# Performance work log

Hardware: AMD Instinct MI355X
Metric: run time of the kernel (lower is better)

The kernel has to match this reference:

```python
import jax, jax.numpy as jnp
import numpy as np

ALPHA = 0.1   # leaky integration rate
NOISE = 0.02  # noise std
B, T, I, H, O = 64, 512, 128, 1024, 64


def setup_inputs() -> dict:
    key = jax.random.key(0)
    k1, k2, k3, k4, k5 = jax.random.split(key, 5)
    x = jax.random.normal(k1, (B, T, I), dtype=jnp.float32)
    wi = jax.random.normal(k2, (I, H), dtype=jnp.float32) / np.sqrt(I).astype(np.float32)
    wrec = jax.random.normal(k3, (H, H), dtype=jnp.float32) / np.sqrt(H).astype(np.float32)
    wo = jax.random.normal(k4, (H, O), dtype=jnp.float32) / np.sqrt(H).astype(np.float32)
    noise = jax.random.normal(k5, (B, T, H), dtype=jnp.float32)  # pre-sampled standard normal
    return {"x": x, "noise": noise, "wi": wi, "wrec": wrec, "wo": wo}


def reference(x, noise, wi, wrec, wo):
    # x: [B,T,I], noise: [B,T,H]; leaky tanh RNN scanned over time.
    batch = x.shape[0]
    h0 = jnp.zeros((batch, wrec.shape[0]), dtype=x.dtype)
    xs = jnp.swapaxes(x, 0, 1)       # [T,B,I]
    ns = jnpp if False else jnp.swapaxes(noise, 0, 1)  # [T,B,H]

    def step(h, inp):
        xt, nt = inp
        h = (1.0 - ALPHA) * h + ALPHA * (xt @ wi + jnp.tanh(h) @ wrec + nt * NOISE)
        return h, jnp.tanh(h) @ wo   # per-step output [B,O]

    _, outs = jax.lax.scan(step, h0, (xs, ns))  # outs: [T,B,O]
    return jnp.swapaxes(outs, 0, 1)  # [B,T,O]
```

## Files before the change

### kernel.cpp

```cpp
#include <hip/hip_runtime.h>
#include <hip/hip_bf16.h>


#define T_ 512
#define I_ 128
#define H_ 1024
#define O_ 64
#define GRPS 8
#define BG 8
#define WPG 32
#define NWG 256
#define POLL_CAP (1<<17)

#define GBUF_ELEMS (GRPS*2*BG*H_)
#define GBUF_BYTES (GBUF_ELEMS*2)
#define STEPFLAG_OFF GBUF_BYTES
#define WS_NEED (GBUF_BYTES + 1024)

#define WREC_HI_E 0
#define WREC_LO_E 32768
#define WI_HI_E   65536
#define WI_LO_E   69632
#define WO_HI_E   73728
#define WO_LO_E   75776
#define RED_OFF_B   155648
#define NOISE_OFF_B 160256
#define LDS_BYTES   161280

typedef __bf16 bf16x8 __attribute__((ext_vector_type(8)));
typedef float f32x4 __attribute__((ext_vector_type(4)));
typedef unsigned u32x4 __attribute__((ext_vector_type(4)));
typedef unsigned short u16;

__device__ __forceinline__ float fast_tanh(float v){
  float cx = fminf(fmaxf(v, -14.f), 14.f);
  float e = __builtin_amdgcn_exp2f(cx * 2.8853900817779268f);
  return 1.f - 2.f * __builtin_amdgcn_rcpf(e + 1.f);
}

__device__ __forceinline__ unsigned sflag_load(const u16* p){
  unsigned v;
  asm volatile("global_load_ushort %0, %1, off sc0 sc1\n\ts_waitcnt vmcnt(0)"
               : "=v"(v) : "v"(p) : "memory");
  return v;
}
__device__ __forceinline__ void sflag_store(u16* p, unsigned v){
  asm volatile("global_store_short %0, %1, off sc0 sc1" :: "v"(p), "v"(v) : "memory");
}
__device__ __forceinline__ void g_load_frag(u32x4& d, const u16* p){
  asm volatile("global_load_dwordx4 %0, %1, off sc0 sc1" : "=v"(d) : "v"(p) : "memory");
}
__device__ __forceinline__ void g_store_u16(u16* p, unsigned v){
  asm volatile("global_store_short %0, %1, off sc0 sc1" :: "v"(p), "v"(v) : "memory");
}

__device__ void load_slice(const float* __restrict__ Wg, int ld, int c0, int K,
                           __bf16* hi, __bf16* lo){
  for (int idx = threadIdx.x; idx < K*32; idx += 256){
    int k = idx >> 5, c = idx & 31;
    float v = Wg[(size_t)k*ld + c0 + c];
    __bf16 h = (__bf16)v;
    __bf16 l = (__bf16)(v - (float)h);
    int kt = k >> 5, kin = k & 31, lg = kin >> 3, j = kin & 7;
    int off = (((kt*2 + (c>>4))*64 + (lg*16 + (c&15))) << 3) + j;
    hi[off] = h; lo[off] = l;
  }
}

#define MFMA __builtin_amdgcn_mfma_f32_16x16x32_bf16
#define BC(u) __builtin_bit_cast(bf16x8, u)

extern "C" __global__ __launch_bounds__(256, 1)
void rnn_kernel(const float* __restrict__ x, const float* __restrict__ noise,
                const float* __restrict__ wi, const float* __restrict__ wrec,
                const float* __restrict__ wo, float* __restrict__ out,
                u16* __restrict__ gbuf, u16* __restrict__ sflags)
{
  extern __shared__ char smem[];
  __bf16* B = (__bf16*)smem;
  float* RED = (float*)(smem + RED_OFF_B);
  float* NS  = (float*)(smem + NOISE_OFF_B);

  const int grp  = blockIdx.x >> 5;
  const int role = blockIdx.x & 31;
  const int c0 = role * 32;

  load_slice(wrec, H_, c0, H_, B + WREC_HI_E, B + WREC_LO_E);
  load_slice(wi,   H_, c0, I_, B + WI_HI_E,  B + WI_LO_E);
  for (int idx = threadIdx.x; idx < 2*H_; idx += 256){
    int col = idx >> 10, k = idx & (H_-1);
    float v = wo[(size_t)k*O_ + role*2 + col];
    __bf16 hh = (__bf16)v;
    B[WO_HI_E + col*H_ + k] = hh;
    B[WO_LO_E + col*H_ + k] = (__bf16)(v - (float)hh);
  }
  __syncthreads();

  const int lane = threadIdx.x & 63;
  const int w    = threadIdx.x >> 6;
  const int lhalf = lane >> 4;
  const int l15   = lane & 15;
  const int bf = lane * 8;

  u16* gg = gbuf + grp * (2*BG*H_);
  u16* gf = sflags + grp * 32;
  const u16* pollp = gf + (lane & 31);
  u16* myflag = gf + role;
  const u16* abase = gg + (size_t)(lane & 7)*H_ + w*256 + lhalf*8;
  const int wo_off = (l15 & 1)*1024 + lhalf*8;

  f32x4 h0 = {0.f,0.f,0.f,0.f};
  f32x4 xA = {0.f,0.f,0.f,0.f}, xB = {0.f,0.f,0.f,0.f};

  for (int i = 0; i < T_; ++i){
    if (w < 2){
      xA = (f32x4){0.f,0.f,0.f,0.f}; xB = (f32x4){0.f,0.f,0.f,0.f};
      const float* xp = x + ((size_t)(grp*BG + (l15 & 7))*T_ + i)*I_ + lhalf*8;
      #pragma unroll
      for (int kt = 0; kt < 4; ++kt){
        f32x4 v0 = *(const f32x4*)(xp + kt*32);
        f32x4 v1 = *(const f32x4*)(xp + kt*32 + 4);
        bf16x8 xh, xl;
        #pragma unroll
        for (int j = 0; j < 4; ++j){
          float a = v0[j], b2 = v1[j];
          __bf16 ah = (__bf16)a, bh2 = (__bf16)b2;
          xh[j] = ah; xh[j+4] = bh2;
          xl[j] = (__bf16)(a - (float)ah); xl[j+4] = (__bf16)(b2 - (float)bh2);
        }
        bf16x8 wih = *(const bf16x8*)(B + WI_HI_E + kt*1024 + w*512 + bf);
        bf16x8 wil = *(const bf16x8*)(B + WI_LO_E + kt*1024 + w*512 + bf);
        xA = MFMA(xh, wih, xA, 0,0,0);
        xB = MFMA(xl, wih, xB, 0,0,0);
        xA = MFMA(xh, wil, xA, 0,0,0);
      }
    } else if (w == 3){
      #pragma unroll
      for (int q = 0; q < 4; ++q){
        int b = (lane>>5) + q*2, c = lane & 31;
        NS[b*32 + c] = noise[((size_t)(grp*BG + b)*T_ + i)*H_ + c0 + c];
      }
    }

    if (i > 0){
      const unsigned tgt = (unsigned)i;
      int guard = 0;
      while (true){
        unsigned v = sflag_load(pollp);
        if (__all((int)(v >= tgt))) break;
        if (++guard > POLL_CAP) break;
      }
    }

    const u16* ap = abase + (size_t)(i & 1)*BG*H_;
    u32x4 a[8];
    #pragma unroll
    for (int kt = 0; kt < 8; ++kt) g_load_frag(a[kt], ap + kt*32);
    asm volatile("s_waitcnt vmcnt(0)"
      : "+v"(a[0]),"+v"(a[1]),"+v"(a[2]),"+v"(a[3]),
        "+v"(a[4]),"+v"(a[5]),"+v"(a[6]),"+v"(a[7]));
    __builtin_amdgcn_sched_barrier(0);

    f32x4 c0A={0.f,0.f,0.f,0.f}, c0B={0.f,0.f,0.f,0.f};
    f32x4 c1A={0.f,0.f,0.f,0.f}, c1B={0.f,0.f,0.f,0.f};
    f32x4 oA ={0.f,0.f,0.f,0.f}, oB ={0.f,0.f,0.f,0.f};
    if (w == 0){ c0A = xA; c0B = xB; }
    if (w == 1){ c1A = xA; c1B = xB; }
    const int kb = w*8;
    #pragma unroll
    for (int kt = 0; kt < 8; ++kt){
      const int kg = kb + kt;
      bf16x8 bh0 = *(const bf16x8*)(B + WREC_HI_E + kg*1024 + bf);
      bf16x8 bl0 = *(const bf16x8*)(B + WREC_LO_E + kg*1024 + bf);
      bf16x8 bh1 = *(const bf16x8*)(B + WREC_HI_E + kg*1024 + 512 + bf);
      bf16x8 bl1 = *(const bf16x8*)(B + WREC_LO_E + kg*1024 + 512 + bf);
      bf16x8 wh  = *(const bf16x8*)(B + WO_HI_E + wo_off + kg*32);
      bf16x8 wl  = *(const bf16x8*)(B + WO_LO_E + wo_off + kg*32);
      bf16x8 av = BC(a[kt]);
      c0A = MFMA(av, bh0, c0A, 0,0,0);  c0B = MFMA(av, bl0, c0B, 0,0,0);
      c1A = MFMA(av, bh1, c1A, 0,0,0);  c1B = MFMA(av, bl1, c1B, 0,0,0);
      oA  = MFMA(av, wh,  oA,  0,0,0);  oB  = MFMA(av, wl,  oB,  0,0,0);
    }
    f32x4 cn0 = c0A + c0B, cn1 = c1A + c1B, co = oA + oB;

    if (lane < 32){
      if (w == 0){ *(f32x4*)&RED[((1*3+0)*32+lane)*4] = cn1; *(f32x4*)&RED[((2*3+0)*32+lane)*4] = co; }
      if (w == 1){ *(f32x4*)&RED[((0*3+0)*32+lane)*4] = cn0; *(f32x4*)&RED[((2*3+1)*32+lane)*4] = co; }
      if (w == 2){ *(f32x4*)&RED[((0*3+1)*32+lane)*4] = cn0; *(f32x4*)&RED[((1*3+1)*32+lane)*4] = cn1; }
      if (w == 3){ *(f32x4*)&RED[((0*3+2)*32+lane)*4] = cn0; *(f32x4*)&RED[((1*3+2)*32+lane)*4] = cn1; *(f32x4*)&RED[((2*3+2)*32+lane)*4] = co; }
    }
    __syncthreads();

    if (w < 2 && lane < 32){
      const int fbase = w ? 1*3 : 0*3;
      f32x4 s = w ? cn1 : cn0;
      s += *(f32x4*)&RED[((fbase+0)*32+lane)*4];
      s += *(f32x4*)&RED[((fbase+1)*32+lane)*4];
      s += *(f32x4*)&RED[((fbase+2)*32+lane)*4];
      u16* gp = gg + (size_t)((i+1)&1)*BG*H_;
      #pragma unroll
      for (int r = 0; r < 4; ++r){
        int row = lhalf*4 + r;
        float hv = 0.9f*h0[r] + 0.1f*s[r] + 0.002f*NS[row*32 + w*16 + l15];
        h0[r] = hv;
        u16 gv = __builtin_bit_cast(u16, (__bf16)fast_tanh(hv));
        g_store_u16(gp + (size_t)row*H_ + c0 + w*16 + l15, (unsigned)gv);
      }
    }
    if (w == 2 && lane < 32 && i > 0){
      f32x4 s = co;
      s += *(f32x4*)&RED[((2*3+0)*32+lane)*4];
      s += *(f32x4*)&RED[((2*3+1)*32+lane)*4];
      s += *(f32x4*)&RED[((2*3+2)*32+lane)*4];
      if (l15 < 2){
        #pragma unroll
        for (int r = 0; r < 4; ++r){
          int row = lhalf*4 + r;
          out[((size_t)(grp*BG + row)*T_ + (i-1))*O_ + role*2 + l15] = s[r];
        }
      }
    }

    asm volatile("s_waitcnt vmcnt(0)" ::: "memory");
    __syncthreads();
    if (threadIdx.x == 0) sflag_store(myflag, (unsigned)(i+1));
  }

  {
    const unsigned tgt = (unsigned)T_;
    int guard = 0;
    while (true){
      unsigned v = sflag_load(pollp);
      if (__all((int)(v >= tgt))) break;
      if (++guard > POLL_CAP) break;
    }
    const u16* ap = abase + (size_t)(T_ & 1)*BG*H_;
    u32x4 a[8];
    #pragma unroll
    for (int kt = 0; kt < 8; ++kt) g_load_frag(a[kt], ap + kt*32);
    asm volatile("s_waitcnt vmcnt(0)"
      : "+v"(a[0]),"+v"(a[1]),"+v"(a[2]),"+v"(a[3]),
        "+v"(a[4]),"+v"(a[5]),"+v"(a[6]),"+v"(a[7]));
    __builtin_amdgcn_sched_barrier(0);
    f32x4 oA={0.f,0.f,0.f,0.f}, oB={0.f,0.f,0.f,0.f};
    const int kb = w*8;
    #pragma unroll
    for (int kt = 0; kt < 8; ++kt){
      const int kg = kb + kt;
      bf16x8 wh = *(const bf16x8*)(B + WO_HI_E + wo_off + kg*32);
      bf16x8 wl = *(const bf16x8*)(B + WO_LO_E + wo_off + kg*32);
      bf16x8 av = BC(a[kt]);
      oA = MFMA(av, wh, oA, 0,0,0);  oB = MFMA(av, wl, oB, 0,0,0);
    }
    f32x4 co = oA + oB;
    if (lane < 32){
      if (w == 0) *(f32x4*)&RED[((2*3+0)*32+lane)*4] = co;
      if (w == 1) *(f32x4*)&RED[((2*3+1)*32+lane)*4] = co;
      if (w == 3) *(f32x4*)&RED[((2*3+2)*32+lane)*4] = co;
    }
    __syncthreads();
    if (w == 2 && lane < 32){
      f32x4 s = co;
      s += *(f32x4*)&RED[((2*3+0)*32+lane)*4];
      s += *(f32x4*)&RED[((2*3+1)*32+lane)*4];
      s += *(f32x4*)&RED[((2*3+2)*32+lane)*4];
      if (l15 < 2){
        #pragma unroll
        for (int r = 0; r < 4; ++r){
          int row = lhalf*4 + r;
          out[((size_t)(grp*BG + row)*T_ + (T_-1))*O_ + role*2 + l15] = s[r];
        }
      }
    }
  }
}

extern "C" void kernel_launch(void* const* d_in, const int* in_sizes, int n_in,
                              void* d_out, int out_size, void* d_ws, size_t ws_size,
                              hipStream_t stream){
  const float* x     = (const float*)d_in[0];
  const float* noise = (const float*)d_in[1];
  const float* wi    = (const float*)d_in[2];
  const float* wrec  = (const float*)d_in[3];
  const float* wo    = (const float*)d_in[4];
  float* out = (float*)d_out;

  if (ws_size < (size_t)WS_NEED) return;
  u16* gbuf = (u16*)d_ws;
  u16* sflags = (u16*)((char*)d_ws + STEPFLAG_OFF);

  hipMemsetAsync(d_ws, 0, WS_NEED, stream);

  hipFuncSetAttribute((const void*)rnn_kernel,
                      hipFuncAttributeMaxDynamicSharedMemorySize, LDS_BYTES);

  void* args[] = {(void*)&x, (void*)&noise, (void*)&wi, (void*)&wrec, (void*)&wo,
                  (void*)&out, (void*)&gbuf, (void*)&sflags};
  hipLaunchCooperativeKernel((const void*)rnn_kernel, dim3(NWG), dim3(256),
                             args, LDS_BYTES, stream);
}
```

Baseline: 3.349 ms.

## Interleave two batch-group chains per workgroup to overlap cross-WG sync latency

Halves the grid to 128 workgroups, each of which now drives two independent 8-row batch groups in alternating half-steps. While one chain computes, the other chain's flag poll, hidden-state fragment loads, x/noise prefetch and input projection are issued, so the global sync latency of one chain is hidden behind the other's work. Flags become per-wave with speculative early polling, and the barriers switch to lgkmcnt-only waits. In exchange each workgroup does twice the MFMA work per step with fewer CUs in use, and the control flow becomes more complex.

```diff
diff --git a/kernel.cpp b/kernel.cpp
--- a/kernel.cpp
+++ b/kernel.cpp
@@ -6,14 +6,10 @@
 #define I_ 128
 #define H_ 1024
 #define O_ 64
-#define GRPS 8
-#define BG 8
-#define WPG 32
-#define NWG 256
+#define NWG 128
 #define POLL_CAP (1<<17)
 
-#define GBUF_ELEMS (GRPS*2*BG*H_)
-#define GBUF_BYTES (GBUF_ELEMS*2)
+#define GBUF_BYTES (8*2*8*H_*2)
 #define STEPFLAG_OFF GBUF_BYTES
 #define WS_NEED (GBUF_BYTES + 1024)
 
@@ -24,8 +20,9 @@
 #define WO_HI_E   73728
 #define WO_LO_E   75776
 #define RED_OFF_B   155648
-#define NOISE_OFF_B 160256
-#define LDS_BYTES   161280
+#define NSA_OFF_B   160256
+#define NSB_OFF_B   161280
+#define LDS_BYTES   162304
 
 typedef __bf16 bf16x8 __attribute__((ext_vector_type(8)));
 typedef float f32x4 __attribute__((ext_vector_type(4)));
@@ -38,6 +35,9 @@
   return 1.f - 2.f * __builtin_amdgcn_rcpf(e + 1.f);
 }
 
+__device__ __forceinline__ void flag_issue(unsigned& v, const u16* p){
+  asm volatile("global_load_ushort %0, %1, off sc0 sc1" : "=v"(v) : "v"(p));
+}
 __device__ __forceinline__ unsigned sflag_load(const u16* p){
   unsigned v;
   asm volatile("global_load_ushort %0, %1, off sc0 sc1\n\ts_waitcnt vmcnt(0)"
@@ -52,6 +52,15 @@
 }
 __device__ __forceinline__ void g_store_u16(u16* p, unsigned v){
   asm volatile("global_store_short %0, %1, off sc0 sc1" :: "v"(p), "v"(v) : "memory");
+}
+__device__ __forceinline__ void gl_f32x4(f32x4& d, const float* p){
+  asm volatile("global_load_dwordx4 %0, %1, off" : "=v"(d) : "v"(p));
+}
+__device__ __forceinline__ void gl_f32(float& d, const float* p){
+  asm volatile("global_load_dword %0, %1, off" : "=v"(d) : "v"(p));
+}
+__device__ __forceinline__ void barrier_lds(){
+  asm volatile("s_waitcnt lgkmcnt(0)\n\ts_barrier" ::: "memory");
 }
 
 __device__ void load_slice(const float* __restrict__ Wg, int ld, int c0, int K,
@@ -70,6 +79,266 @@
 #define MFMA __builtin_amdgcn_mfma_f32_16x16x32_bf16
 #define BC(u) __builtin_bit_cast(bf16x8, u)
 
+struct Chain {
+  u32x4 a[8];
+  f32x4 h0, xA, xB;
+  u16 *gg, *gf;
+  const u16 *ab;
+  const float *xb, *nb;
+  float *ob;
+  float *NS;
+};
+
+__device__ __forceinline__ void do_half(
+    Chain& C, Chain& D, int i, int j,
+    __bf16* B, float* RED,
+    int lane, int w, int lhalf, int l15, int bf, int wo_off, int c0, int role)
+{
+  asm volatile("s_waitcnt vmcnt(0)"
+    : "+v"(C.a[0]),"+v"(C.a[1]),"+v"(C.a[2]),"+v"(C.a[3]),
+      "+v"(C.a[4]),"+v"(C.a[5]),"+v"(C.a[6]),"+v"(C.a[7]) :: "memory");
+  __builtin_amdgcn_sched_barrier(0);
+
+  f32x4 xv0,xv1,xv2,xv3,xv4,xv5,xv6,xv7;
+  float n0,n1,n2,n3;
+  if (j < T_){
+    if (w < 2){
+      const float* xp = D.xb + ((size_t)(l15 & 7)*T_ + (size_t)j)*I_ + lhalf*8;
+      gl_f32x4(xv0, xp);      gl_f32x4(xv1, xp+4);
+      gl_f32x4(xv2, xp+32);   gl_f32x4(xv3, xp+36);
+      gl_f32x4(xv4, xp+64);   gl_f32x4(xv5, xp+68);
+      gl_f32x4(xv6, xp+96);   gl_f32x4(xv7, xp+100);
+    } else if (w == 3){
+      const int b0 = lane >> 5, cc = lane & 31;
+      gl_f32(n0, D.nb + ((size_t)(b0+0)*T_ + j)*H_ + c0 + cc);
+      gl_f32(n1, D.nb + ((size_t)(b0+2)*T_ + j)*H_ + c0 + cc);
+      gl_f32(n2, D.nb + ((size_t)(b0+4)*T_ + j)*H_ + c0 + cc);
+      gl_f32(n3, D.nb + ((size_t)(b0+6)*T_ + j)*H_ + c0 + cc);
+    }
+  }
+  unsigned pv; flag_issue(pv, D.gf + lane);
+
+  f32x4 c0A={0.f,0.f,0.f,0.f}, c0B={0.f,0.f,0.f,0.f};
+  f32x4 c1A={0.f,0.f,0.f,0.f}, c1B={0.f,0.f,0.f,0.f};
+  f32x4 oA ={0.f,0.f,0.f,0.f}, oB ={0.f,0.f,0.f,0.f};
+  if (w == 0){ c0A = C.xA; c0B = C.xB; }
+  if (w == 1){ c1A = C.xA; c1B = C.xB; }
+  const int kb = w*8;
+  #pragma unroll
+  for (int kt = 0; kt < 8; ++kt){
+    const int kg = kb + kt;
+    bf16x8 bh0 = *(const bf16x8*)(B + WREC_HI_E + kg*1024 + bf);
+    bf16x8 bl0 = *(const bf16x8*)(B + WREC_LO_E + kg*1024 + bf);
+    bf16x8 bh1 = *(const bf16x8*)(B + WREC_HI_E + kg*1024 + 512 + bf);
+    bf16x8 bl1 = *(const bf16x8*)(B + WREC_LO_E + kg*1024 + 512 + bf);
+    bf16x8 wh  = *(const bf16x8*)(B + WO_HI_E + wo_off + kg*32);
+    bf16x8 wl  = *(const bf16x8*)(B + WO_LO_E + wo_off + kg*32);
+    bf16x8 av = BC(C.a[kt]);
+    c0A = MFMA(av, bh0, c0A, 0,0,0);  c0B = MFMA(av, bl0, c0B, 0,0,0);
+    c1A = MFMA(av, bh1, c1A, 0,0,0);  c1B = MFMA(av, bl1, c1B, 0,0,0);
+    oA  = MFMA(av, wh,  oA,  0,0,0);  oB  = MFMA(av, wl,  oB,  0,0,0);
+  }
+  f32x4 cn0 = c0A + c0B, cn1 = c1A + c1B, co = oA + oB;
+
+  if (lane < 32){
+    if (w == 0){ *(f32x4*)&RED[((1*3+0)*32+lane)*4] = cn1; *(f32x4*)&RED[((2*3+0)*32+lane)*4] = co; }
+    if (w == 1){ *(f32x4*)&RED[((0*3+0)*32+lane)*4] = cn0; *(f32x4*)&RED[((2*3+1)*32+lane)*4] = co; }
+    if (w == 2){ *(f32x4*)&RED[((0*3+1)*32+lane)*4] = cn0; *(f32x4*)&RED[((1*3+1)*32+lane)*4] = cn1; }
+    if (w == 3){ *(f32x4*)&RED[((0*3+2)*32+lane)*4] = cn0; *(f32x4*)&RED[((1*3+2)*32+lane)*4] = cn1; *(f32x4*)&RED[((2*3+2)*32+lane)*4] = co; }
+  }
+  barrier_lds();
+
+  if (w < 2 && lane < 32){
+    const int fbase = w ? 3 : 0;
+    f32x4 s = w ? cn1 : cn0;
+    s += *(f32x4*)&RED[((fbase+0)*32+lane)*4];
+    s += *(f32x4*)&RED[((fbase+1)*32+lane)*4];
+    s += *(f32x4*)&RED[((fbase+2)*32+lane)*4];
+    u16* gp = C.gg + (size_t)((i+1)&1)*(8*H_);
+    #pragma unroll
+    for (int r = 0; r < 4; ++r){
+      int row = lhalf*4 + r;
+      float hv = 0.9f*C.h0[r] + 0.1f*s[r] + 0.002f*C.NS[row*32 + w*16 + l15];
+      C.h0[r] = hv;
+      u16 gv = __builtin_bit_cast(u16, (__bf16)fast_tanh(hv));
+      g_store_u16(gp + (size_t)row*H_ + c0 + w*16 + l15, (unsigned)gv);
+    }
+  }
+  if (w == 2 && lane < 32 && i > 0){
+    f32x4 s = co;
+    s += *(f32x4*)&RED[((2*3+0)*32+lane)*4];
+    s += *(f32x4*)&RED[((2*3+1)*32+lane)*4];
+    s += *(f32x4*)&RED[((2*3+2)*32+lane)*4];
+    if (l15 < 2){
+      #pragma unroll
+      for (int r = 0; r < 4; ++r){
+        int row = lhalf*4 + r;
+        C.ob[((size_t)row*T_ + (i-1))*O_ + role*2 + l15] = s[r];
+      }
+    }
+  }
+
+  if (j < T_ && w < 2){
+    asm volatile("s_waitcnt vmcnt(0)"
+      : "+v"(pv),"+v"(xv0),"+v"(xv1),"+v"(xv2),"+v"(xv3),
+        "+v"(xv4),"+v"(xv5),"+v"(xv6),"+v"(xv7) :: "memory");
+  } else if (j < T_ && w == 3){
+    asm volatile("s_waitcnt vmcnt(0)"
+      : "+v"(pv),"+v"(n0),"+v"(n1),"+v"(n2),"+v"(n3) :: "memory");
+  } else {
+    asm volatile("s_waitcnt vmcnt(0)" : "+v"(pv) :: "memory");
+  }
+  __builtin_amdgcn_sched_barrier(0);
+
+  if (w < 2 && lane == 0) sflag_store(C.gf + role*2 + w, (unsigned)(i+1));
+
+  {
+    const unsigned tgt = (unsigned)j;
+    if (!__all((int)(pv >= tgt))){
+      int guard = 0;
+      while (true){
+        unsigned v = sflag_load(D.gf + lane);
+        if (__all((int)(v >= tgt))) break;
+        if (++guard > POLL_CAP) break;
+      }
+    }
+  }
+  {
+    const u16* ap = D.ab + (size_t)(j & 1)*(8*H_);
+    #pragma unroll
+    for (int kt = 0; kt < 8; ++kt) g_load_frag(D.a[kt], ap + kt*32);
+  }
+  if (j < T_){
+    if (w < 2){
+      f32x4 nxA = {0.f,0.f,0.f,0.f}, nxB = {0.f,0.f,0.f,0.f};
+      #pragma unroll
+      for (int kt = 0; kt < 4; ++kt){
+        f32x4 v0 = (kt==0)?xv0:(kt==1)?xv2:(kt==2)?xv4:xv6;
+        f32x4 v1 = (kt==0)?xv1:(kt==1)?xv3:(kt==2)?xv5:xv7;
+        bf16x8 xh, xl;
+        #pragma unroll
+        for (int jj = 0; jj < 4; ++jj){
+          float aa = v0[jj], bb = v1[jj];
+          __bf16 ah = (__bf16)aa, bh2 = (__bf16)bb;
+          xh[jj] = ah; xh[jj+4] = bh2;
+          xl[jj] = (__bf16)(aa - (float)ah); xl[jj+4] = (__bf16)(bb - (float)bh2);
+        }
+        bf16x8 wih = *(const bf16x8*)(B + WI_HI_E + kt*1024 + w*512 + bf);
+        bf16x8 wil = *(const bf16x8*)(B + WI_LO_E + kt*1024 + w*512 + bf);
+        nxA = MFMA(xh, wih, nxA, 0,0,0);
+        nxB = MFMA(xl, wih, nxB, 0,0,0);
+        nxA = MFMA(xh, wil, nxA, 0,0,0);
+      }
+      D.xA = nxA; D.xB = nxB;
+    } else if (w == 3){
+      const int b0 = lane >> 5, cc = lane & 31;
+      D.NS[(b0+0)*32 + cc] = n0;
+      D.NS[(b0+2)*32 + cc] = n1;
+      D.NS[(b0+4)*32 + cc] = n2;
+      D.NS[(b0+6)*32 + cc] = n3;
+    }
+  }
+
+  barrier_lds();
+}
+
+__device__ __forceinline__ void prep0(Chain& D, __bf16* B,
+    int lane, int w, int lhalf, int l15, int bf, int c0)
+{
+  f32x4 xv0,xv1,xv2,xv3,xv4,xv5,xv6,xv7;
+  float n0,n1,n2,n3;
+  if (w < 2){
+    const float* xp = D.xb + (size_t)(l15 & 7)*T_*I_ + lhalf*8;
+    gl_f32x4(xv0, xp);      gl_f32x4(xv1, xp+4);
+    gl_f32x4(xv2, xp+32);   gl_f32x4(xv3, xp+36);
+    gl_f32x4(xv4, xp+64);   gl_f32x4(xv5, xp+68);
+    gl_f32x4(xv6, xp+96);   gl_f32x4(xv7, xp+100);
+    asm volatile("s_waitcnt vmcnt(0)"
+      : "+v"(xv0),"+v"(xv1),"+v"(xv2),"+v"(xv3),
+        "+v"(xv4),"+v"(xv5),"+v"(xv6),"+v"(xv7) :: "memory");
+  } else if (w == 3){
+    const int b0 = lane >> 5, cc = lane & 31;
+    gl_f32(n0, D.nb + (size_t)(b0+0)*T_*H_ + c0 + cc);
+    gl_f32(n1, D.nb + (size_t)(b0+2)*T_*H_ + c0 + cc);
+    gl_f32(n2, D.nb + (size_t)(b0+4)*T_*H_ + c0 + cc);
+    gl_f32(n3, D.nb + (size_t)(b0+6)*T_*H_ + c0 + cc);
+    asm volatile("s_waitcnt vmcnt(0)"
+      : "+v"(n0),"+v"(n1),"+v"(n2),"+v"(n3) :: "memory");
+  }
+  __builtin_amdgcn_sched_barrier(0);
+  #pragma unroll
+  for (int kt = 0; kt < 8; ++kt) g_load_frag(D.a[kt], D.ab + kt*32);
+  if (w < 2){
+    f32x4 nxA = {0.f,0.f,0.f,0.f}, nxB = {0.f,0.f,0.f,0.f};
+    #pragma unroll
+    for (int kt = 0; kt < 4; ++kt){
+      f32x4 v0 = (kt==0)?xv0:(kt==1)?xv2:(kt==2)?xv4:xv6;
+      f32x4 v1 = (kt==0)?xv1:(kt==1)?xv3:(kt==2)?xv5:xv7;
+      bf16x8 xh, xl;
+      #pragma unroll
+      for (int jj = 0; jj < 4; ++jj){
+        float aa = v0[jj], bb = v1[jj];
+        __bf16 ah = (__bf16)aa, bh2 = (__bf16)bb;
+        xh[jj] = ah; xh[jj+4] = bh2;
+        xl[jj] = (__bf16)(aa - (float)ah); xl[jj+4] = (__bf16)(bb - (float)bh2);
+      }
+      bf16x8 wih = *(const bf16x8*)(B + WI_HI_E + kt*1024 + w*512 + bf);
+      bf16x8 wil = *(const bf16x8*)(B + WI_LO_E + kt*1024 + w*512 + bf);
+      nxA = MFMA(xh, wih, nxA, 0,0,0);
+      nxB = MFMA(xl, wih, nxB, 0,0,0);
+      nxA = MFMA(xh, wil, nxA, 0,0,0);
+    }
+    D.xA = nxA; D.xB = nxB;
+  } else if (w == 3){
+    const int b0 = lane >> 5, cc = lane & 31;
+    D.NS[(b0+0)*32 + cc] = n0;
+    D.NS[(b0+2)*32 + cc] = n1;
+    D.NS[(b0+4)*32 + cc] = n2;
+    D.NS[(b0+6)*32 + cc] = n3;
+  }
+  barrier_lds();
+}
+
+__device__ __forceinline__ void epi(Chain& C, __bf16* B, float* RED,
+    int lane, int w, int lhalf, int l15, int bf, int wo_off, int role)
+{
+  asm volatile("s_waitcnt vmcnt(0)"
+    : "+v"(C.a[0]),"+v"(C.a[1]),"+v"(C.a[2]),"+v"(C.a[3]),
+      "+v"(C.a[4]),"+v"(C.a[5]),"+v"(C.a[6]),"+v"(C.a[7]) :: "memory");
+  __builtin_amdgcn_sched_barrier(0);
+  f32x4 oA={0.f,0.f,0.f,0.f}, oB={0.f,0.f,0.f,0.f};
+  const int kb = w*8;
+  #pragma unroll
+  for (int kt = 0; kt < 8; ++kt){
+    const int kg = kb + kt;
+    bf16x8 wh = *(const bf16x8*)(B + WO_HI_E + wo_off + kg*32);
+    bf16x8 wl = *(const bf16x8*)(B + WO_LO_E + wo_off + kg*32);
+    bf16x8 av = BC(C.a[kt]);
+    oA = MFMA(av, wh, oA, 0,0,0);  oB = MFMA(av, wl, oB, 0,0,0);
+  }
+  f32x4 co = oA + oB;
+  barrier_lds();
+  if (lane < 32){
+    if (w == 0) *(f32x4*)&RED[((2*3+0)*32+lane)*4] = co;
+    if (w == 1) *(f32x4*)&RED[((2*3+1)*32+lane)*4] = co;
+    if (w == 3) *(f32x4*)&RED[((2*3+2)*32+lane)*4] = co;
+  }
+  barrier_lds();
+  if (w == 2 && lane < 32){
+    f32x4 s = co;
+    s += *(f32x4*)&RED[((2*3+0)*32+lane)*4];
+    s += *(f32x4*)&RED[((2*3+1)*32+lane)*4];
+    s += *(f32x4*)&RED[((2*3+2)*32+lane)*4];
+    if (l15 < 2){
+      #pragma unroll
+      for (int r = 0; r < 4; ++r){
+        int row = lhalf*4 + r;
+        C.ob[((size_t)row*T_ + (T_-1))*O_ + role*2 + l15] = s[r];
+      }
+    }
+  }
+}
+
 extern "C" __global__ __launch_bounds__(256, 1)
 void rnn_kernel(const float* __restrict__ x, const float* __restrict__ noise,
                 const float* __restrict__ wi, const float* __restrict__ wrec,
@@ -79,9 +348,8 @@
   extern __shared__ char smem[];
   __bf16* B = (__bf16*)smem;
   float* RED = (float*)(smem + RED_OFF_B);
-  float* NS  = (float*)(smem + NOISE_OFF_B);
-
-  const int grp  = blockIdx.x >> 5;
+
+  const int pid  = blockIdx.x >> 5;
   const int role = blockIdx.x & 31;
   const int c0 = role * 32;
 
@@ -101,178 +369,41 @@
   const int lhalf = lane >> 4;
   const int l15   = lane & 15;
   const int bf = lane * 8;
-
-  u16* gg = gbuf + grp * (2*BG*H_);
-  u16* gf = sflags + grp * 32;
-  const u16* pollp = gf + (lane & 31);
-  u16* myflag = gf + role;
-  const u16* abase = gg + (size_t)(lane & 7)*H_ + w*256 + lhalf*8;
   const int wo_off = (l15 & 1)*1024 + lhalf*8;
 
-  f32x4 h0 = {0.f,0.f,0.f,0.f};
-  f32x4 xA = {0.f,0.f,0.f,0.f}, xB = {0.f,0.f,0.f,0.f};
+  Chain A, Bc;
+  const int gA = pid*2, gB = pid*2+1;
+  A.gg  = gbuf + gA*(2*8*H_);   A.gf  = sflags + gA*64;
+  Bc.gg = gbuf + gB*(2*8*H_);   Bc.gf = sflags + gB*64;
+  A.ab  = A.gg  + (size_t)(lane & 7)*H_ + w*256 + lhalf*8;
+  Bc.ab = Bc.gg + (size_t)(lane & 7)*H_ + w*256 + lhalf*8;
+  A.xb  = x + (size_t)(gA*8)*T_*I_;     Bc.xb = x + (size_t)(gB*8)*T_*I_;
+  A.nb  = noise + (size_t)(gA*8)*T_*H_; Bc.nb = noise + (size_t)(gB*8)*T_*H_;
+  A.ob  = out + (size_t)(gA*8)*T_*O_;   Bc.ob = out + (size_t)(gB*8)*T_*O_;
+  A.NS  = (float*)(smem + NSA_OFF_B);   Bc.NS = (float*)(smem + NSB_OFF_B);
+  A.h0  = (f32x4){0.f,0.f,0.f,0.f};     Bc.h0 = (f32x4){0.f,0.f,0.f,0.f};
+  A.xA  = (f32x4){0.f,0.f,0.f,0.f};     A.xB  = (f32x4){0.f,0.f,0.f,0.f};
+  Bc.xA = (f32x4){0.f,0.f,0.f,0.f};     Bc.xB = (f32x4){0.f,0.f,0.f,0.f};
+
+  prep0(A, B, lane, w, lhalf, l15, bf, c0);
 
   for (int i = 0; i < T_; ++i){
-    if (w < 2){
-      xA = (f32x4){0.f,0.f,0.f,0.f}; xB = (f32x4){0.f,0.f,0.f,0.f};
-      const float* xp = x + ((size_t)(grp*BG + (l15 & 7))*T_ + i)*I_ + lhalf*8;
-      #pragma unroll
-      for (int kt = 0; kt < 4; ++kt){
-        f32x4 v0 = *(const f32x4*)(xp + kt*32);
-        f32x4 v1 = *(const f32x4*)(xp + kt*32 + 4);
-        bf16x8 xh, xl;
-        #pragma unroll
-        for (int j = 0; j < 4; ++j){
-          float a = v0[j], b2 = v1[j];
-          __bf16 ah = (__bf16)a, bh2 = (__bf16)b2;
-          xh[j] = ah; xh[j+4] = bh2;
-          xl[j] = (__bf16)(a - (float)ah); xl[j+4] = (__bf16)(b2 - (float)bh2);
-        }
-        bf16x8 wih = *(const bf16x8*)(B + WI_HI_E + kt*1024 + w*512 + bf);
-        bf16x8 wil = *(const bf16x8*)(B + WI_LO_E + kt*1024 + w*512 + bf);
-        xA = MFMA(xh, wih, xA, 0,0,0);
-        xB = MFMA(xl, wih, xB, 0,0,0);
-        xA = MFMA(xh, wil, xA, 0,0,0);
-      }
-    } else if (w == 3){
-      #pragma unroll
-      for (int q = 0; q < 4; ++q){
-        int b = (lane>>5) + q*2, c = lane & 31;
-        NS[b*32 + c] = noise[((size_t)(grp*BG + b)*T_ + i)*H_ + c0 + c];
-      }
-    }
-
-    if (i > 0){
-      const unsigned tgt = (unsigned)i;
-      int guard = 0;
-      while (true){
-        unsigned v = sflag_load(pollp);
-        if (__all((int)(v >= tgt))) break;
-        if (++guard > POLL_CAP) break;
-      }
-    }
-
-    const u16* ap = abase + (size_t)(i & 1)*BG*H_;
-    u32x4 a[8];
-    #pragma unroll
-    for (int kt = 0; kt < 8; ++kt) g_load_frag(a[kt], ap + kt*32);
-    asm volatile("s_waitcnt vmcnt(0)"
-      : "+v"(a[0]),"+v"(a[1]),"+v"(a[2]),"+v"(a[3]),
-        "+v"(a[4]),"+v"(a[5]),"+v"(a[6]),"+v"(a[7]));
-    __builtin_amdgcn_sched_barrier(0);
-
-    f32x4 c0A={0.f,0.f,0.f,0.f}, c0B={0.f,0.f,0.f,0.f};
-    f32x4 c1A={0.f,0.f,0.f,0.f}, c1B={0.f,0.f,0.f,0.f};
-    f32x4 oA ={0.f,0.f,0.f,0.f}, oB ={0.f,0.f,0.f,0.f};
-    if (w == 0){ c0A = xA; c0B = xB; }
-    if (w == 1){ c1A = xA; c1B = xB; }
-    const int kb = w*8;
-    #pragma unroll
-    for (int kt = 0; kt < 8; ++kt){
-      const int kg = kb + kt;
-      bf16x8 bh0 = *(const bf16x8*)(B + WREC_HI_E + kg*1024 + bf);
-      bf16x8 bl0 = *(const bf16x8*)(B + WREC_LO_E + kg*1024 + bf);
-      bf16x8 bh1 = *(const bf16x8*)(B + WREC_HI_E + kg*1024 + 512 + bf);
-      bf16x8 bl1 = *(const bf16x8*)(B + WREC_LO_E + kg*1024 + 512 + bf);
-      bf16x8 wh  = *(const bf16x8*)(B + WO_HI_E + wo_off + kg*32);
-      bf16x8 wl  = *(const bf16x8*)(B + WO_LO_E + wo_off + kg*32);
-      bf16x8 av = BC(a[kt]);
-      c0A = MFMA(av, bh0, c0A, 0,0,0);  c0B = MFMA(av, bl0, c0B, 0,0,0);
-      c1A = MFMA(av, bh1, c1A, 0,0,0);  c1B = MFMA(av, bl1, c1B, 0,0,0);
-      oA  = MFMA(av, wh,  oA,  0,0,0);  oB  = MFMA(av, wl,  oB,  0,0,0);
-    }
-    f32x4 cn0 = c0A + c0B, cn1 = c1A + c1B, co = oA + oB;
-
-    if (lane < 32){
-      if (w == 0){ *(f32x4*)&RED[((1*3+0)*32+lane)*4] = cn1; *(f32x4*)&RED[((2*3+0)*32+lane)*4] = co; }
-      if (w == 1){ *(f32x4*)&RED[((0*3+0)*32+lane)*4] = cn0; *(f32x4*)&RED[((2*3+1)*32+lane)*4] = co; }
-      if (w == 2){ *(f32x4*)&RED[((0*3+1)*32+lane)*4] = cn0; *(f32x4*)&RED[((1*3+1)*32+lane)*4] = cn1; }
-      if (w == 3){ *(f32x4*)&RED[((0*3+2)*32+lane)*4] = cn0; *(f32x4*)&RED[((1*3+2)*32+lane)*4] = cn1; *(f32x4*)&RED[((2*3+2)*32+lane)*4] = co; }
-    }
-    __syncthreads();
-
-    if (w < 2 && lane < 32){
-      const int fbase = w ? 1*3 : 0*3;
-      f32x4 s = w ? cn1 : cn0;
-      s += *(f32x4*)&RED[((fbase+0)*32+lane)*4];
-      s += *(f32x4*)&RED[((fbase+1)*32+lane)*4];
-      s += *(f32x4*)&RED[((fbase+2)*32+lane)*4];
-      u16* gp = gg + (size_t)((i+1)&1)*BG*H_;
-      #pragma unroll
-      for (int r = 0; r < 4; ++r){
-        int row = lhalf*4 + r;
-        float hv = 0.9f*h0[r] + 0.1f*s[r] + 0.002f*NS[row*32 + w*16 + l15];
-        h0[r] = hv;
-        u16 gv = __builtin_bit_cast(u16, (__bf16)fast_tanh(hv));
-        g_store_u16(gp + (size_t)row*H_ + c0 + w*16 + l15, (unsigned)gv);
-      }
-    }
-    if (w == 2 && lane < 32 && i > 0){
-      f32x4 s = co;
-      s += *(f32x4*)&RED[((2*3+0)*32+lane)*4];
-      s += *(f32x4*)&RED[((2*3+1)*32+lane)*4];
-      s += *(f32x4*)&RED[((2*3+2)*32+lane)*4];
-      if (l15 < 2){
-        #pragma unroll
-        for (int r = 0; r < 4; ++r){
-          int row = lhalf*4 + r;
-          out[((size_t)(grp*BG + row)*T_ + (i-1))*O_ + role*2 + l15] = s[r];
-        }
-      }
-    }
-
-    asm volatile("s_waitcnt vmcnt(0)" ::: "memory");
-    __syncthreads();
-    if (threadIdx.x == 0) sflag_store(myflag, (unsigned)(i+1));
-  }
-
+    do_half(A,  Bc, i, i,   B, RED, lane, w, lhalf, l15, bf, wo_off, c0, role);
+    do_half(Bc, A,  i, i+1, B, RED, lane, w, lhalf, l15, bf, wo_off, c0, role);
+  }
+
+  epi(A, B, RED, lane, w, lhalf, l15, bf, wo_off, role);
   {
-    const unsigned tgt = (unsigned)T_;
     int guard = 0;
     while (true){
-      unsigned v = sflag_load(pollp);
-      if (__all((int)(v >= tgt))) break;
+      unsigned v = sflag_load(Bc.gf + lane);
+      if (__all((int)(v >= (unsigned)T_))) break;
       if (++guard > POLL_CAP) break;
     }
-    const u16* ap = abase + (size_t)(T_ & 1)*BG*H_;
-    u32x4 a[8];
     #pragma unroll
-    for (int kt = 0; kt < 8; ++kt) g_load_frag(a[kt], ap + kt*32);
-    asm volatile("s_waitcnt vmcnt(0)"
-      : "+v"(a[0]),"+v"(a[1]),"+v"(a[2]),"+v"(a[3]),
-        "+v"(a[4]),"+v"(a[5]),"+v"(a[6]),"+v"(a[7]));
-    __builtin_amdgcn_sched_barrier(0);
-    f32x4 oA={0.f,0.f,0.f,0.f}, oB={0.f,0.f,0.f,0.f};
-    const int kb = w*8;
-    #pragma unroll
-    for (int kt = 0; kt < 8; ++kt){
-      const int kg = kb + kt;
-      bf16x8 wh = *(const bf16x8*)(B + WO_HI_E + wo_off + kg*32);
-      bf16x8 wl = *(const bf16x8*)(B + WO_LO_E + wo_off + kg*32);
-      bf16x8 av = BC(a[kt]);
-      oA = MFMA(av, wh, oA, 0,0,0);  oB = MFMA(av, wl, oB, 0,0,0);
-    }
-    f32x4 co = oA + oB;
-    if (lane < 32){
-      if (w == 0) *(f32x4*)&RED[((2*3+0)*32+lane)*4] = co;
-      if (w == 1) *(f32x4*)&RED[((2*3+1)*32+lane)*4] = co;
-      if (w == 3) *(f32x4*)&RED[((2*3+2)*32+lane)*4] = co;
-    }
-    __syncthreads();
-    if (w == 2 && lane < 32){
-      f32x4 s = co;
-      s += *(f32x4*)&RED[((2*3+0)*32+lane)*4];
-      s += *(f32x4*)&RED[((2*3+1)*32+lane)*4];
-      s += *(f32x4*)&RED[((2*3+2)*32+lane)*4];
-      if (l15 < 2){
-        #pragma unroll
-        for (int r = 0; r < 4; ++r){
-          int row = lhalf*4 + r;
-          out[((size_t)(grp*BG + row)*T_ + (T_-1))*O_ + role*2 + l15] = s[r];
-        }
-      }
-    }
-  }
+    for (int kt = 0; kt < 8; ++kt) g_load_frag(Bc.a[kt], Bc.ab + kt*32);
+  }
+  epi(Bc, B, RED, lane, w, lhalf, l15, bf, wo_off, role);
 }
 
 extern "C" void kernel_launch(void* const* d_in, const int* in_sizes, int n_in,
```

Result: faster. 3.036 ms (-9.3%).

## Use 16-row batch groups and prefetch inputs across the step barrier

Applied to the files above, without the earlier changes.

Halves the number of workgroups by processing 16 batch rows per group, so each MFMA uses all 16 M-rows instead of 8. Input x and noise are prefetched one to two steps ahead into registers, and the next step's input projection is computed while waiting on the flags. The single per-block flag and full block barriers are replaced by per-wave flags and lightweight LDS barriers, and the h fragment loads are waited on progressively per k-tile. The aim is to cut per-step synchronization latency and underutilized MFMA work, at the cost of fewer active CUs and more register pressure.

```diff
diff --git a/kernel.cpp b/kernel.cpp
--- a/kernel.cpp
+++ b/kernel.cpp
@@ -6,14 +6,13 @@
 #define I_ 128
 #define H_ 1024
 #define O_ 64
-#define GRPS 8
-#define BG 8
+#define GRPS 4
+#define BG 16
 #define WPG 32
-#define NWG 256
+#define NWG 128
 #define POLL_CAP (1<<17)
 
-#define GBUF_ELEMS (GRPS*2*BG*H_)
-#define GBUF_BYTES (GBUF_ELEMS*2)
+#define GBUF_BYTES (GRPS*2*BG*H_*2)
 #define STEPFLAG_OFF GBUF_BYTES
 #define WS_NEED (GBUF_BYTES + 1024)
 
@@ -23,9 +22,9 @@
 #define WI_LO_E   69632
 #define WO_HI_E   73728
 #define WO_LO_E   75776
-#define RED_OFF_B   155648
-#define NOISE_OFF_B 160256
-#define LDS_BYTES   161280
+#define RED_B     155648
+#define REDO_B    161792
+#define LDS_BYTES 162176
 
 typedef __bf16 bf16x8 __attribute__((ext_vector_type(8)));
 typedef float f32x4 __attribute__((ext_vector_type(4)));
@@ -38,6 +37,9 @@
   return 1.f - 2.f * __builtin_amdgcn_rcpf(e + 1.f);
 }
 
+__device__ __forceinline__ void flag_issue(unsigned& v, const u16* p){
+  asm volatile("global_load_ushort %0, %1, off sc0 sc1" : "=v"(v) : "v"(p));
+}
 __device__ __forceinline__ unsigned sflag_load(const u16* p){
   unsigned v;
   asm volatile("global_load_ushort %0, %1, off sc0 sc1\n\ts_waitcnt vmcnt(0)"
@@ -48,10 +50,22 @@
   asm volatile("global_store_short %0, %1, off sc0 sc1" :: "v"(p), "v"(v) : "memory");
 }
 __device__ __forceinline__ void g_load_frag(u32x4& d, const u16* p){
-  asm volatile("global_load_dwordx4 %0, %1, off sc0 sc1" : "=v"(d) : "v"(p) : "memory");
+  asm volatile("global_load_dwordx4 %0, %1, off sc0 sc1" : "=v"(d) : "v"(p));
 }
 __device__ __forceinline__ void g_store_u16(u16* p, unsigned v){
   asm volatile("global_store_short %0, %1, off sc0 sc1" :: "v"(p), "v"(v) : "memory");
+}
+__device__ __forceinline__ void g_store_f32(float* p, float v){
+  asm volatile("global_store_dword %0, %1, off" :: "v"(p), "v"(v) : "memory");
+}
+__device__ __forceinline__ void gl_f32x4(f32x4& d, const float* p){
+  asm volatile("global_load_dwordx4 %0, %1, off" : "=v"(d) : "v"(p));
+}
+__device__ __forceinline__ void gl_f32(float& d, const float* p){
+  asm volatile("global_load_dword %0, %1, off" : "=v"(d) : "v"(p));
+}
+__device__ __forceinline__ void barrier_lds(){
+  asm volatile("s_waitcnt lgkmcnt(0)\n\ts_barrier" ::: "memory");
 }
 
 __device__ void load_slice(const float* __restrict__ Wg, int ld, int c0, int K,
@@ -70,6 +84,15 @@
 #define MFMA __builtin_amdgcn_mfma_f32_16x16x32_bf16
 #define BC(u) __builtin_bit_cast(bf16x8, u)
 
+#define PACKX(v0, v1, xh, xl)                                      \
+  { _Pragma("unroll")                                              \
+    for (int jj = 0; jj < 4; ++jj){                                \
+      float aa = (v0)[jj], bb = (v1)[jj];                          \
+      __bf16 ah = (__bf16)aa, bh2 = (__bf16)bb;                    \
+      (xh)[jj] = ah; (xh)[jj+4] = bh2;                             \
+      (xl)[jj] = (__bf16)(aa - (float)ah);                         \
+      (xl)[jj+4] = (__bf16)(bb - (float)bh2); } }
+
 extern "C" __global__ __launch_bounds__(256, 1)
 void rnn_kernel(const float* __restrict__ x, const float* __restrict__ noise,
                 const float* __restrict__ wi, const float* __restrict__ wrec,
@@ -78,8 +101,8 @@
 {
   extern __shared__ char smem[];
   __bf16* B = (__bf16*)smem;
-  float* RED = (float*)(smem + RED_OFF_B);
-  float* NS  = (float*)(smem + NOISE_OFF_B);
+  float* REDN = (float*)(smem + RED_B);
+  float* REDO = (float*)(smem + REDO_B);
 
   const int grp  = blockIdx.x >> 5;
   const int role = blockIdx.x & 31;
@@ -101,147 +124,175 @@
   const int lhalf = lane >> 4;
   const int l15   = lane & 15;
   const int bf = lane * 8;
+  const int wo_off = (l15 & 1)*1024 + lhalf*8;
 
   u16* gg = gbuf + grp * (2*BG*H_);
-  u16* gf = sflags + grp * 32;
-  const u16* pollp = gf + (lane & 31);
-  u16* myflag = gf + role;
-  const u16* abase = gg + (size_t)(lane & 7)*H_ + w*256 + lhalf*8;
-  const int wo_off = (l15 & 1)*1024 + lhalf*8;
+  u16* gf = sflags + grp * 64;
+  const u16* pollp = gf + lane;
+  const u16* abase = gg + (size_t)l15*H_ + w*256 + lhalf*8;
+
+  const float* xrow  = x + (size_t)(grp*BG + l15)*T_*I_ + lhalf*8;
+  const float* nrow0 = noise + (size_t)(grp*BG + lhalf*4)*T_*H_ + c0 + (w&1)*16 + l15;
+  float* orow = out + (size_t)(grp*BG + lhalf*4)*T_*O_ + role*2 + (l15 & 1);
 
   f32x4 h0 = {0.f,0.f,0.f,0.f};
   f32x4 xA = {0.f,0.f,0.f,0.f}, xB = {0.f,0.f,0.f,0.f};
+  u32x4 a[8];
+  f32x4 xv[8];
+  float nz[4] = {0.f,0.f,0.f,0.f};
+
+  if (w < 2){
+    gl_f32x4(xv[0], xrow);      gl_f32x4(xv[1], xrow+4);
+    gl_f32x4(xv[2], xrow+32);   gl_f32x4(xv[3], xrow+36);
+    gl_f32x4(xv[4], xrow+64);   gl_f32x4(xv[5], xrow+68);
+    gl_f32x4(xv[6], xrow+96);   gl_f32x4(xv[7], xrow+100);
+    asm volatile("s_waitcnt vmcnt(0)"
+      : "+v"(xv[0]),"+v"(xv[1]),"+v"(xv[2]),"+v"(xv[3]),
+        "+v"(xv[4]),"+v"(xv[5]),"+v"(xv[6]),"+v"(xv[7]));
+    __builtin_amdgcn_sched_barrier(0);
+    #pragma unroll
+    for (int kt = 0; kt < 4; ++kt){
+      bf16x8 xh, xl; PACKX(xv[kt*2], xv[kt*2+1], xh, xl);
+      bf16x8 wih = *(const bf16x8*)(B + WI_HI_E + kt*1024 + w*512 + bf);
+      bf16x8 wil = *(const bf16x8*)(B + WI_LO_E + kt*1024 + w*512 + bf);
+      xA = MFMA(xh, wih, xA, 0,0,0);
+      xB = MFMA(xl, wih, xB, 0,0,0);
+      xA = MFMA(xh, wil, xA, 0,0,0);
+    }
+    const float* xp = xrow + I_;
+    gl_f32x4(xv[0], xp);      gl_f32x4(xv[1], xp+4);
+    gl_f32x4(xv[2], xp+32);   gl_f32x4(xv[3], xp+36);
+    gl_f32x4(xv[4], xp+64);   gl_f32x4(xv[5], xp+68);
+    gl_f32x4(xv[6], xp+96);   gl_f32x4(xv[7], xp+100);
+    gl_f32(nz[0], nrow0);
+    gl_f32(nz[1], nrow0 + (size_t)T_*H_);
+    gl_f32(nz[2], nrow0 + (size_t)2*T_*H_);
+    gl_f32(nz[3], nrow0 + (size_t)3*T_*H_);
+  }
+  #pragma unroll
+  for (int kt = 0; kt < 8; ++kt) g_load_frag(a[kt], abase + kt*32);
 
   for (int i = 0; i < T_; ++i){
-    if (w < 2){
-      xA = (f32x4){0.f,0.f,0.f,0.f}; xB = (f32x4){0.f,0.f,0.f,0.f};
-      const float* xp = x + ((size_t)(grp*BG + (l15 & 7))*T_ + i)*I_ + lhalf*8;
-      #pragma unroll
-      for (int kt = 0; kt < 4; ++kt){
-        f32x4 v0 = *(const f32x4*)(xp + kt*32);
-        f32x4 v1 = *(const f32x4*)(xp + kt*32 + 4);
-        bf16x8 xh, xl;
-        #pragma unroll
-        for (int j = 0; j < 4; ++j){
-          float a = v0[j], b2 = v1[j];
-          __bf16 ah = (__bf16)a, bh2 = (__bf16)b2;
-          xh[j] = ah; xh[j+4] = bh2;
-          xl[j] = (__bf16)(a - (float)ah); xl[j+4] = (__bf16)(b2 - (float)bh2);
-        }
-        bf16x8 wih = *(const bf16x8*)(B + WI_HI_E + kt*1024 + w*512 + bf);
-        bf16x8 wil = *(const bf16x8*)(B + WI_LO_E + kt*1024 + w*512 + bf);
-        xA = MFMA(xh, wih, xA, 0,0,0);
-        xB = MFMA(xl, wih, xB, 0,0,0);
-        xA = MFMA(xh, wil, xA, 0,0,0);
-      }
-    } else if (w == 3){
-      #pragma unroll
-      for (int q = 0; q < 4; ++q){
-        int b = (lane>>5) + q*2, c = lane & 31;
-        NS[b*32 + c] = noise[((size_t)(grp*BG + b)*T_ + i)*H_ + c0 + c];
-      }
-    }
-
-    if (i > 0){
-      const unsigned tgt = (unsigned)i;
-      int guard = 0;
-      while (true){
-        unsigned v = sflag_load(pollp);
-        if (__all((int)(v >= tgt))) break;
-        if (++guard > POLL_CAP) break;
-      }
-    }
-
-    const u16* ap = abase + (size_t)(i & 1)*BG*H_;
-    u32x4 a[8];
-    #pragma unroll
-    for (int kt = 0; kt < 8; ++kt) g_load_frag(a[kt], ap + kt*32);
-    asm volatile("s_waitcnt vmcnt(0)"
-      : "+v"(a[0]),"+v"(a[1]),"+v"(a[2]),"+v"(a[3]),
-        "+v"(a[4]),"+v"(a[5]),"+v"(a[6]),"+v"(a[7]));
-    __builtin_amdgcn_sched_barrier(0);
-
     f32x4 c0A={0.f,0.f,0.f,0.f}, c0B={0.f,0.f,0.f,0.f};
     f32x4 c1A={0.f,0.f,0.f,0.f}, c1B={0.f,0.f,0.f,0.f};
     f32x4 oA ={0.f,0.f,0.f,0.f}, oB ={0.f,0.f,0.f,0.f};
     if (w == 0){ c0A = xA; c0B = xB; }
     if (w == 1){ c1A = xA; c1B = xB; }
     const int kb = w*8;
-    #pragma unroll
-    for (int kt = 0; kt < 8; ++kt){
-      const int kg = kb + kt;
-      bf16x8 bh0 = *(const bf16x8*)(B + WREC_HI_E + kg*1024 + bf);
-      bf16x8 bl0 = *(const bf16x8*)(B + WREC_LO_E + kg*1024 + bf);
-      bf16x8 bh1 = *(const bf16x8*)(B + WREC_HI_E + kg*1024 + 512 + bf);
-      bf16x8 bl1 = *(const bf16x8*)(B + WREC_LO_E + kg*1024 + 512 + bf);
-      bf16x8 wh  = *(const bf16x8*)(B + WO_HI_E + wo_off + kg*32);
-      bf16x8 wl  = *(const bf16x8*)(B + WO_LO_E + wo_off + kg*32);
-      bf16x8 av = BC(a[kt]);
-      c0A = MFMA(av, bh0, c0A, 0,0,0);  c0B = MFMA(av, bl0, c0B, 0,0,0);
-      c1A = MFMA(av, bh1, c1A, 0,0,0);  c1B = MFMA(av, bl1, c1B, 0,0,0);
-      oA  = MFMA(av, wh,  oA,  0,0,0);  oB  = MFMA(av, wl,  oB,  0,0,0);
-    }
+#define CSTEP(KT, N)                                                          \
+    { asm volatile("s_waitcnt vmcnt(" #N ")" : "+v"(a[KT]));                  \
+      __builtin_amdgcn_sched_barrier(0);                                      \
+      const int kg = kb + KT;                                                 \
+      bf16x8 av = BC(a[KT]);                                                  \
+      bf16x8 bh0 = *(const bf16x8*)(B + WREC_HI_E + kg*1024 + bf);            \
+      bf16x8 bl0 = *(const bf16x8*)(B + WREC_LO_E + kg*1024 + bf);            \
+      bf16x8 bh1 = *(const bf16x8*)(B + WREC_HI_E + kg*1024 + 512 + bf);      \
+      bf16x8 bl1 = *(const bf16x8*)(B + WREC_LO_E + kg*1024 + 512 + bf);      \
+      bf16x8 wh  = *(const bf16x8*)(B + WO_HI_E + wo_off + kg*32);            \
+      bf16x8 wl  = *(const bf16x8*)(B + WO_LO_E + wo_off + kg*32);            \
+      c0A = MFMA(av, bh0, c0A, 0,0,0);  c0B = MFMA(av, bl0, c0B, 0,0,0);      \
+      c1A = MFMA(av, bh1, c1A, 0,0,0);  c1B = MFMA(av, bl1, c1B, 0,0,0);      \
+      oA  = MFMA(av, wh,  oA,  0,0,0);  oB  = MFMA(av, wl,  oB,  0,0,0); }
+    CSTEP(0,7) CSTEP(1,6) CSTEP(2,5) CSTEP(3,4)
+    CSTEP(4,3) CSTEP(5,2) CSTEP(6,1) CSTEP(7,0)
+#undef CSTEP
     f32x4 cn0 = c0A + c0B, cn1 = c1A + c1B, co = oA + oB;
 
-    if (lane < 32){
-      if (w == 0){ *(f32x4*)&RED[((1*3+0)*32+lane)*4] = cn1; *(f32x4*)&RED[((2*3+0)*32+lane)*4] = co; }
-      if (w == 1){ *(f32x4*)&RED[((0*3+0)*32+lane)*4] = cn0; *(f32x4*)&RED[((2*3+1)*32+lane)*4] = co; }
-      if (w == 2){ *(f32x4*)&RED[((0*3+1)*32+lane)*4] = cn0; *(f32x4*)&RED[((1*3+1)*32+lane)*4] = cn1; }
-      if (w == 3){ *(f32x4*)&RED[((0*3+2)*32+lane)*4] = cn0; *(f32x4*)&RED[((1*3+2)*32+lane)*4] = cn1; *(f32x4*)&RED[((2*3+2)*32+lane)*4] = co; }
-    }
-    __syncthreads();
-
-    if (w < 2 && lane < 32){
-      const int fbase = w ? 1*3 : 0*3;
+    if (w == 0){ *(f32x4*)&REDN[((1*3+0)*64+lane)*4] = cn1;
+                 if (l15 < 2) *(f32x4*)&REDO[(0*8 + lhalf*2 + l15)*4] = co; }
+    if (w == 1){ *(f32x4*)&REDN[((0*3+0)*64+lane)*4] = cn0;
+                 if (l15 < 2) *(f32x4*)&REDO[(1*8 + lhalf*2 + l15)*4] = co; }
+    if (w == 2){ *(f32x4*)&REDN[((0*3+1)*64+lane)*4] = cn0;
+                 *(f32x4*)&REDN[((1*3+1)*64+lane)*4] = cn1; }
+    if (w == 3){ *(f32x4*)&REDN[((0*3+2)*64+lane)*4] = cn0;
+                 *(f32x4*)&REDN[((1*3+2)*64+lane)*4] = cn1;
+                 if (l15 < 2) *(f32x4*)&REDO[(2*8 + lhalf*2 + l15)*4] = co; }
+    barrier_lds();
+
+    if (w < 2){
+      const int fb = w ? 3 : 0;
       f32x4 s = w ? cn1 : cn0;
-      s += *(f32x4*)&RED[((fbase+0)*32+lane)*4];
-      s += *(f32x4*)&RED[((fbase+1)*32+lane)*4];
-      s += *(f32x4*)&RED[((fbase+2)*32+lane)*4];
-      u16* gp = gg + (size_t)((i+1)&1)*BG*H_;
+      s += *(f32x4*)&REDN[((fb+0)*64+lane)*4];
+      s += *(f32x4*)&REDN[((fb+1)*64+lane)*4];
+      s += *(f32x4*)&REDN[((fb+2)*64+lane)*4];
+      u16* gp = gg + (size_t)((i+1)&1)*(BG*H_);
       #pragma unroll
       for (int r = 0; r < 4; ++r){
         int row = lhalf*4 + r;
-        float hv = 0.9f*h0[r] + 0.1f*s[r] + 0.002f*NS[row*32 + w*16 + l15];
+        float hv = 0.9f*h0[r] + 0.1f*s[r] + 0.002f*nz[r];
         h0[r] = hv;
         u16 gv = __builtin_bit_cast(u16, (__bf16)fast_tanh(hv));
         g_store_u16(gp + (size_t)row*H_ + c0 + w*16 + l15, (unsigned)gv);
       }
-    }
-    if (w == 2 && lane < 32 && i > 0){
+    } else if (w == 2 && i > 0 && l15 < 2){
       f32x4 s = co;
-      s += *(f32x4*)&RED[((2*3+0)*32+lane)*4];
-      s += *(f32x4*)&RED[((2*3+1)*32+lane)*4];
-      s += *(f32x4*)&RED[((2*3+2)*32+lane)*4];
-      if (l15 < 2){
-        #pragma unroll
-        for (int r = 0; r < 4; ++r){
-          int row = lhalf*4 + r;
-          out[((size_t)(grp*BG + row)*T_ + (i-1))*O_ + role*2 + l15] = s[r];
-        }
-      }
-    }
-
-    asm volatile("s_waitcnt vmcnt(0)" ::: "memory");
-    __syncthreads();
-    if (threadIdx.x == 0) sflag_store(myflag, (unsigned)(i+1));
-  }
-
+      s += *(f32x4*)&REDO[(0*8 + lhalf*2 + l15)*4];
+      s += *(f32x4*)&REDO[(1*8 + lhalf*2 + l15)*4];
+      s += *(f32x4*)&REDO[(2*8 + lhalf*2 + l15)*4];
+      #pragma unroll
+      for (int r = 0; r < 4; ++r)
+        g_store_f32(orow + (size_t)r*T_*O_ + (size_t)(i-1)*O_, s[r]);
+    }
+
+    if (w < 2){
+      asm volatile("s_waitcnt vmcnt(0)" ::: "memory");
+      if (lane == 0) sflag_store(gf + role*2 + w, (unsigned)(i+1));
+    }
+
+    unsigned pv;
+    flag_issue(pv, pollp);
+    if (w < 2 && i+1 < T_){
+      f32x4 nxA = {0.f,0.f,0.f,0.f}, nxB = {0.f,0.f,0.f,0.f};
+      #pragma unroll
+      for (int kt = 0; kt < 4; ++kt){
+        bf16x8 xh, xl; PACKX(xv[kt*2], xv[kt*2+1], xh, xl);
+        bf16x8 wih = *(const bf16x8*)(B + WI_HI_E + kt*1024 + w*512 + bf);
+        bf16x8 wil = *(const bf16x8*)(B + WI_LO_E + kt*1024 + w*512 + bf);
+        nxA = MFMA(xh, wih, nxA, 0,0,0);
+        nxB = MFMA(xl, wih, nxB, 0,0,0);
+        nxA = MFMA(xh, wil, nxA, 0,0,0);
+      }
+      xA = nxA; xB = nxB;
+    }
+    asm volatile("s_waitcnt vmcnt(0)" : "+v"(pv));
+    __builtin_amdgcn_sched_barrier(0);
+    if (!__all((int)(pv >= (unsigned)(i+1)))){
+      int guard = 0;
+      while (true){
+        unsigned v = sflag_load(pollp);
+        if (__all((int)(v >= (unsigned)(i+1)))) break;
+        if (++guard > POLL_CAP) break;
+      }
+    }
+    if (w < 2){
+      if (i+2 < T_){
+        const float* xp = xrow + (size_t)(i+2)*I_;
+        gl_f32x4(xv[0], xp);      gl_f32x4(xv[1], xp+4);
+        gl_f32x4(xv[2], xp+32);   gl_f32x4(xv[3], xp+36);
+        gl_f32x4(xv[4], xp+64);   gl_f32x4(xv[5], xp+68);
+        gl_f32x4(xv[6], xp+96);   gl_f32x4(xv[7], xp+100);
+      }
+      if (i+1 < T_){
+        const float* np = nrow0 + (size_t)(i+1)*H_;
+        gl_f32(nz[0], np);
+        gl_f32(nz[1], np + (size_t)T_*H_);
+        gl_f32(nz[2], np + (size_t)2*T_*H_);
+        gl_f32(nz[3], np + (size_t)3*T_*H_);
+      }
+    }
+    {
+      const u16* ap = abase + (size_t)((i+1)&1)*(BG*H_);
+      #pragma unroll
+      for (int kt = 0; kt < 8; ++kt) g_load_frag(a[kt], ap + kt*32);
+    }
+    barrier_lds();
+  }
+
+  asm volatile("s_waitcnt vmcnt(0)"
+    : "+v"(a[0]),"+v"(a[1]),"+v"(a[2]),"+v"(a[3]),
+      "+v"(a[4]),"+v"(a[5]),"+v"(a[6]),"+v"(a[7]));
+  __builtin_amdgcn_sched_barrier(0);
   {
-    const unsigned tgt = (unsigned)T_;
-    int guard = 0;
-    while (true){
-      unsigned v = sflag_load(pollp);
-      if (__all((int)(v >= tgt))) break;
-      if (++guard > POLL_CAP) break;
-    }
-    const u16* ap = abase + (size_t)(T_ & 1)*BG*H_;
-    u32x4 a[8];
-    #pragma unroll
-    for (int kt = 0; kt < 8; ++kt) g_load_frag(a[kt], ap + kt*32);
-    asm volatile("s_waitcnt vmcnt(0)"
-      : "+v"(a[0]),"+v"(a[1]),"+v"(a[2]),"+v"(a[3]),
-        "+v"(a[4]),"+v"(a[5]),"+v"(a[6]),"+v"(a[7]));
-    __builtin_amdgcn_sched_barrier(0);
     f32x4 oA={0.f,0.f,0.f,0.f}, oB={0.f,0.f,0.f,0.f};
     const int kb = w*8;
     #pragma unroll
@@ -253,26 +304,23 @@
       oA = MFMA(av, wh, oA, 0,0,0);  oB = MFMA(av, wl, oB, 0,0,0);
     }
     f32x4 co = oA + oB;
-    if (lane < 32){
-      if (w == 0) *(f32x4*)&RED[((2*3+0)*32+lane)*4] = co;
-      if (w == 1) *(f32x4*)&RED[((2*3+1)*32+lane)*4] = co;
-      if (w == 3) *(f32x4*)&RED[((2*3+2)*32+lane)*4] = co;
-    }
-    __syncthreads();
-    if (w == 2 && lane < 32){
+    if (l15 < 2){
+      if (w == 0) *(f32x4*)&REDO[(0*8 + lhalf*2 + l15)*4] = co;
+      if (w == 1) *(f32x4*)&REDO[(1*8 + lhalf*2 + l15)*4] = co;
+      if (w == 3) *(f32x4*)&REDO[(2*8 + lhalf*2 + l15)*4] = co;
+    }
+    barrier_lds();
+    if (w == 2 && l15 < 2){
       f32x4 s = co;
-      s += *(f32x4*)&RED[((2*3+0)*32+lane)*4];
-      s += *(f32x4*)&RED[((2*3+1)*32+lane)*4];
-      s += *(f32x4*)&RED[((2*3+2)*32+lane)*4];
-      if (l15 < 2){
-        #pragma unroll
-        for (int r = 0; r < 4; ++r){
-          int row = lhalf*4 + r;
-          out[((size_t)(grp*BG + row)*T_ + (T_-1))*O_ + role*2 + l15] = s[r];
-        }
-      }
-    }
-  }
+      s += *(f32x4*)&REDO[(0*8 + lhalf*2 + l15)*4];
+      s += *(f32x4*)&REDO[(1*8 + lhalf*2 + l15)*4];
+      s += *(f32x4*)&REDO[(2*8 + lhalf*2 + l15)*4];
+      #pragma unroll
+      for (int r = 0; r < 4; ++r)
+        g_store_f32(orow + (size_t)r*T_*O_ + (size_t)(T_-1)*O_, s[r]);
+    }
+  }
+  asm volatile("s_waitcnt vmcnt(0)" ::: "memory");
 }
 
 extern "C" void kernel_launch(void* const* d_in, const int* in_sizes, int n_in,
```

After: 3.193 ms. 4.6% less time.
